# Kernel optimization log

Hardware: AMD Instinct MI355X
Metric: run time of the kernel (lower is better)

## Reference

```python
import jax, jax.numpy as jnp
import numpy as np

B, C, H, W = 2, 14, 128, 128
LOSS_WEIGHT = 0.5  # output = (1 - loss_weight) * sum of per-(bs,cls) log-Hausdorff losses
BIG = 1e6          # 'infinite' 1D distance for columns with no background pixel


def _edt_sq(is_zero):
    """Exact squared Euclidean distance transform of a [H,W] bool map.

    Returns, for every pixel, the squared distance to the nearest True pixel
    of `is_zero` (0 at True pixels). Matches scipy.ndimage.distance_transform_edt
    squared. Two-phase separable brute force (vectorized, no data loops).
    """
    h, w = is_zero.shape
    ii = jnp.arange(h, dtype=jnp.float32)
    absd = jnp.abs(ii[:, None] - ii[None, :])  # [H(i), H(p)] = |i - p|
    # d1[i, q] = min_{p : is_zero[p, q]} |i - p|   (per-column 1D distance)
    d1 = jnp.min(jnp.where(is_zero[None, :, :], absd[:, :, None], BIG), axis=1)  # [H, W]
    jj = jnp.arange(w, dtype=jnp.float32)
    off = (jj[:, None] - jj[None, :]) ** 2  # [W(q), W(j)] = (q - j)^2
    # sq[i, j] = min_q d1[i, q]^2 + (q - j)^2
    return jnp.min(d1[:, :, None] ** 2 + off[None, :, :], axis=1)  # [H, W]


def _distance_field_sq(img):
    """MONAI HausdorffDTLoss.distance_field squared: (edt(fg)+edt(bg))^2.

    fg_dist and bg_dist have disjoint supports, so (fg+bg)^2 = fg^2 + bg^2.
    Zero field if the image is all-foreground or all-background.
    """
    fg = img > 0.5
    field = _edt_sq(~fg) + _edt_sq(fg)
    valid = jnp.any(fg) & jnp.any(~fg)
    return jnp.where(valid, field, 0.0)


def _edge_mask(m):
    """mask XOR binary_erosion(mask): scipy default cross structuring element,
    border_value=0 (borders erode)."""
    p = jnp.pad(m, 1, constant_values=False)
    er = m & p[:-2, 1:-1] & p[2:, 1:-1] & p[1:-1, :-2] & p[1:-1, 2:]
    return m & ~er


def _pair_loss(stud_logit, seg_s, seg_t, teach_pred):
    # stud_logit: [H,W] float logits of this class; seg_s/seg_t: [H,W] bool
    # class masks; teach_pred: [H,W] teacher argmax labels (int)
    es = _edge_mask(seg_s).astype(stud_logit.dtype)
    et = _edge_mask(seg_t)
    pred = es * stud_logit                                      # edges * logits
    targ = jnp.where(et, teach_pred.astype(stud_logit.dtype), 0.0)  # edges * labels
    pred_dt2 = jax.lax.stop_gradient(_distance_field_sq(pred))  # MONAI detaches dt
    targ_dt2 = jax.lax.stop_gradient(_distance_field_sq(targ))
    hd = jnp.mean((pred - targ) ** 2 * (pred_dt2 + targ_dt2))   # alpha = 2
    return jnp.log(hd + 1.0)                                    # LogHausdorffDTLoss


def reference(logits_student, logits_teacher):
    ps = jnp.argmax(logits_student, axis=1)  # softmax is monotone -> argmax of logits
    pt = jnp.argmax(logits_teacher, axis=1)
    cls = jnp.arange(1, C)                   # classes 1..C-1 (background skipped)
    n = B * (C - 1)
    seg_s = (ps[:, None] == cls[None, :, None, None]).reshape(n, H, W)
    seg_t = (pt[:, None] == cls[None, :, None, None]).reshape(n, H, W)
    stud = logits_student[:, 1:].reshape(n, H, W)
    pt_rep = jnp.broadcast_to(pt[:, None], (B, C - 1, H, W)).reshape(n, H, W)
    losses = jax.vmap(_pair_loss)(stud, seg_s, seg_t, pt_rep)
    return (1.0 - LOSS_WEIGHT) * jnp.sum(losses)


def setup_inputs() -> dict:
    key = jax.random.key(0)
    k1, k2 = jax.random.split(key)
    return {
        "logits_student": jax.random.normal(k1, (B, C, H, W), dtype=jnp.float32),
        "logits_teacher": jax.random.normal(k2, (B, C, H, W), dtype=jnp.float32),
    }
```

## Files before the change

kernel.cpp:

```cpp
#include <hip/hip_runtime.h>
#include <math.h>
#include <limits.h>

#define HH 128
#define WW 128
#define HW (HH*WW)
#define BB 2
#define CC 14
#define NPAIR 26
#define RPB 8
#define NBLK (NPAIR * (HH / RPB))

typedef unsigned long long u64;


__device__ inline int nbd(u64 lo, u64 hi, int i) {
    int up = 255, down = 255;
    u64 slo, shi;
    if (i == 0)      { slo = lo; shi = hi; }
    else if (i < 64) { slo = (lo >> i) | (hi << (64 - i)); shi = hi >> i; }
    else             { slo = hi >> (i - 64); shi = 0ULL; }
    if (slo)      up = __builtin_ctzll(slo);
    else if (shi) up = 64 + __builtin_ctzll(shi);
    int s = 127 - i;
    u64 llo, lhi;
    if (s == 0)      { llo = lo; lhi = hi; }
    else if (s < 64) { lhi = (hi << s) | (lo >> (64 - s)); llo = lo << s; }
    else             { lhi = lo << (s - 64); llo = 0ULL; }
    if (lhi)      down = __builtin_clzll(lhi);
    else if (llo) down = 64 + __builtin_clzll(llo);
    return min(up, down);
}

__global__ void k_argmax(const float* __restrict__ Ls, const float* __restrict__ Lt,
                         unsigned char* __restrict__ lab, unsigned short* __restrict__ hb,
                         float* __restrict__ sums, int* __restrict__ done) {
    if (blockIdx.x == 0) {
        if (threadIdx.x < NPAIR) sums[threadIdx.x] = 0.0f;
        if (threadIdx.x == 0) *done = 0;
    }
    int p4 = blockIdx.x * blockDim.x + threadIdx.x;
    if (p4 >= BB * HW / 4) return;
    int b = p4 >> 12;
    int q4 = p4 & (HW / 4 - 1);
    const float4* bs = (const float4*)(Ls + (size_t)b * CC * HW) + q4;
    const float4* bt = (const float4*)(Lt + (size_t)b * CC * HW) + q4;
    float4 mS = bs[0], mT = bt[0];
    uchar4 iS = make_uchar4(0, 0, 0, 0), iT = make_uchar4(0, 0, 0, 0);
    ushort4 hm = make_ushort4(0, 0, 0, 0);
#pragma unroll
    for (int c = 1; c < CC; ++c) {
        float4 v = bs[(size_t)c * (HW / 4)];
        if (v.x > mS.x) { mS.x = v.x; iS.x = (unsigned char)c; }
        if (v.y > mS.y) { mS.y = v.y; iS.y = (unsigned char)c; }
        if (v.z > mS.z) { mS.z = v.z; iS.z = (unsigned char)c; }
        if (v.w > mS.w) { mS.w = v.w; iS.w = (unsigned char)c; }
        unsigned short bit = (unsigned short)(1u << (c - 1));
        if (v.x > 0.5f) hm.x |= bit;
        if (v.y > 0.5f) hm.y |= bit;
        if (v.z > 0.5f) hm.z |= bit;
        if (v.w > 0.5f) hm.w |= bit;
        float4 u = bt[(size_t)c * (HW / 4)];
        if (u.x > mT.x) { mT.x = u.x; iT.x = (unsigned char)c; }
        if (u.y > mT.y) { mT.y = u.y; iT.y = (unsigned char)c; }
        if (u.z > mT.z) { mT.z = u.z; iT.z = (unsigned char)c; }
        if (u.w > mT.w) { mT.w = u.w; iT.w = (unsigned char)c; }
    }
    uchar4 pk = make_uchar4((unsigned char)(iS.x | (iT.x << 4)),
                            (unsigned char)(iS.y | (iT.y << 4)),
                            (unsigned char)(iS.z | (iT.z << 4)),
                            (unsigned char)(iS.w | (iT.w << 4)));
    ((uchar4*)lab)[b * (HW / 4) + q4] = pk;
    ((ushort4*)hb)[b * (HW / 4) + q4] = hm;
}

__device__ inline u64 asm64(unsigned int (*p)[WW], int k0, int j) {
    return (u64)p[k0][j] | ((u64)p[k0 + 1][j] << 16)
         | ((u64)p[k0 + 2][j] << 32) | ((u64)p[k0 + 3][j] << 48);
}

__global__ __launch_bounds__(1024) void k_C(
        const unsigned char* __restrict__ lab, const unsigned short* __restrict__ hb,
        const float* __restrict__ Ls,
        float* __restrict__ sums, int* __restrict__ done, float* __restrict__ out) {
    int n = blockIdx.x >> 4;
    int t = blockIdx.x & 15;
    int tid = threadIdx.x;
    int k = tid >> 7;
    int j = tid & (WW - 1);
    int b = n / (CC - 1), c = 1 + (n - b * (CC - 1));
    const unsigned char*  LB = lab + b * HW;
    const unsigned short* HB = hb + b * HW;
    const float* Lp = Ls + (size_t)(b * CC + c) * HW;

    int i = t * RPB + k;
    float lv = Lp[i * WW + j];

    unsigned int s16 = 0, t16 = 0, h16 = 0;
    int i0 = k << 4;
    unsigned int hbit = 1u << (c - 1);
#pragma unroll
    for (int r = 0; r < 16; ++r) {
        int off = (i0 + r) * WW + j;
        unsigned int lbv = LB[off];
        if ((lbv & 15u) == (unsigned)c)  s16 |= 1u << r;
        if ((lbv >> 4)  == (unsigned)c)  t16 |= 1u << r;
        if (HB[off] & hbit)              h16 |= 1u << r;
    }
    __shared__ unsigned int pS[8][WW], pT[8][WW], pH[8][WW];
    pS[k][j] = s16; pT[k][j] = t16; pH[k][j] = h16;
    __syncthreads();

    __shared__ ulonglong2 colFP[WW], colET[WW], colES[WW];
    __shared__ int sfl[2];
    if (tid < WW) {
        u64 ms0 = asm64(pS, 0, j), ms1 = asm64(pS, 4, j);
        u64 mt0 = asm64(pT, 0, j), mt1 = asm64(pT, 4, j);
        u64 hi0 = asm64(pH, 0, j), hi1 = asm64(pH, 4, j);
        u64 Lsx = 0, Lsy = 0, Ltx = 0, Lty = 0, Rsx = 0, Rsy = 0, Rtx = 0, Rty = 0;
        if (j > 0)      { Lsx = asm64(pS, 0, j - 1); Lsy = asm64(pS, 4, j - 1);
                          Ltx = asm64(pT, 0, j - 1); Lty = asm64(pT, 4, j - 1); }
        if (j < WW - 1) { Rsx = asm64(pS, 0, j + 1); Rsy = asm64(pS, 4, j + 1);
                          Rtx = asm64(pT, 0, j + 1); Rty = asm64(pT, 4, j + 1); }

        u64 U0 = ms0 << 1, U1 = (ms1 << 1) | (ms0 >> 63);
        u64 D0 = (ms0 >> 1) | (ms1 << 63), D1 = ms1 >> 1;
        u64 er0 = ms0 & U0 & D0 & Lsx & Rsx;
        u64 er1 = ms1 & U1 & D1 & Lsy & Rsy;
        u64 es0 = ms0 & ~er0, es1 = ms1 & ~er1;

        u64 Ut0 = mt0 << 1, Ut1 = (mt1 << 1) | (mt0 >> 63);
        u64 Dt0 = (mt0 >> 1) | (mt1 << 63), Dt1 = mt1 >> 1;
        u64 ert0 = mt0 & Ut0 & Dt0 & Ltx & Rtx;
        u64 ert1 = mt1 & Ut1 & Dt1 & Lty & Rty;
        u64 et0 = mt0 & ~ert0, et1 = mt1 & ~ert1;

        u64 fp0 = es0 & hi0, fp1 = es1 & hi1;

        colFP[j] = make_ulonglong2(fp0, fp1);
        colET[j] = make_ulonglong2(et0, et1);
        colES[j] = make_ulonglong2(es0, es1);

        u64 bFgP = __ballot((fp0 | fp1) != 0ull);
        u64 bBgP = __ballot((fp0 & fp1) != ~0ull);
        u64 bFgT = __ballot((et0 | et1) != 0ull);
        u64 bBgT = __ballot((et0 & et1) != ~0ull);
        if ((tid & 63) == 0) {
            sfl[tid >> 6] = (bFgP ? 1 : 0) | (bBgP ? 2 : 0)
                          | (bFgT ? 4 : 0) | (bBgT ? 8 : 0);
        }
    }
    __syncthreads();

    ulonglong2 mP = colFP[j];
    ulonglong2 mT = colET[j];
    ulonglong2 eS = colES[j];
    int f = sfl[0] | sfl[1];
    bool aP = (f & 3) == 3, aT = (f & 12) == 12;

    int dP  = nbd(mP.x, mP.y, i);
    int dPb = nbd(~mP.x, ~mP.y, i);
    int dT  = nbd(mT.x, mT.y, i);
    int dTb = nbd(~mT.x, ~mT.y, i);

    __shared__ uchar4 sq[RPB][WW];
    sq[k][j] = make_uchar4((unsigned char)dP, (unsigned char)dPb,
                           (unsigned char)dT, (unsigned char)dTb);
    __syncthreads();

    int bP = dP * dP, bPb = dPb * dPb, bT = dT * dT, bTb = dTb * dTb;
    int need = 0;
    if (aP) need = max(bP, bPb);
    if (aT) need = max(need, max(bT, bTb));
    for (int rad = 1; rad < WW; ++rad) {
        int rr = rad * rad;
        if (rr >= need) break;
        if (j >= rad) {
            uchar4 s = sq[k][j - rad];
            bP  = min(bP,  (int)s.x * s.x + rr); bPb = min(bPb, (int)s.y * s.y + rr);
            bT  = min(bT,  (int)s.z * s.z + rr); bTb = min(bTb, (int)s.w * s.w + rr);
        }
        if (j + rad < WW) {
            uchar4 s = sq[k][j + rad];
            bP  = min(bP,  (int)s.x * s.x + rr); bPb = min(bPb, (int)s.y * s.y + rr);
            bT  = min(bT,  (int)s.z * s.z + rr); bTb = min(bTb, (int)s.w * s.w + rr);
        }
        need = 0;
        if (aP) need = max(bP, bPb);
        if (aT) need = max(need, max(bT, bTb));
    }

    float fieldP = aP ? (float)(bP + bPb) : 0.0f;
    float fieldT = aT ? (float)(bT + bTb) : 0.0f;

    bool es = ((i < 64 ? (eS.x >> i) : (eS.y >> (i - 64))) & 1ull) != 0;
    bool et = ((i < 64 ? (mT.x >> i) : (mT.y >> (i - 64))) & 1ull) != 0;
    float predv = es ? lv : 0.0f;
    float targv = et ? (float)c : 0.0f;
    float diff = predv - targv;
    float v = diff * diff * (fieldP + fieldT);

    for (int o = 32; o > 0; o >>= 1) v += __shfl_down(v, o);
    __shared__ float wsum[16];
    __shared__ int won;
    int lane = tid & 63, w = tid >> 6;
    if (lane == 0) wsum[w] = v;
    if (tid == 0) won = 0;
    __syncthreads();
    if (tid == 0) {
        float tot = 0.0f;
#pragma unroll
        for (int q = 0; q < 16; ++q) tot += wsum[q];
        atomicAdd(&sums[n], tot);
        __threadfence();
        if (atomicAdd(done, 1) == NBLK - 1) won = 1;
    }
    __syncthreads();
    if (won && tid < 64) {
        float vv = 0.0f;
        if (tid < NPAIR) {
            float hd = atomicAdd(&sums[tid], 0.0f) * (1.0f / (float)HW);
            vv = logf(hd + 1.0f);
        }
        for (int o = 32; o > 0; o >>= 1) vv += __shfl_down(vv, o);
        if (tid == 0) out[0] = 0.5f * vv;
    }
}

extern "C" void kernel_launch(void* const* d_in, const int* in_sizes, int n_in,
                              void* d_out, int out_size, void* d_ws, size_t ws_size,
                              hipStream_t stream) {
    const float* Ls = (const float*)d_in[0];
    const float* Lt = (const float*)d_in[1];
    float* out = (float*)d_out;

    char* w = (char*)d_ws;
    unsigned char*  lab  = (unsigned char*) (w);
    unsigned short* hbm  = (unsigned short*)(w + 32768);
    float*          sums = (float*)         (w + 98304);
    int*            done = (int*)           (w + 98432);

    k_argmax<<<BB * HW / 4 / 256, 256, 0, stream>>>(Ls, Lt, lab, hbm, sums, done);
    k_C<<<NBLK, 1024, 0, stream>>>(lab, hbm, Ls, sums, done, out);
}
```

Before: 72.09 us.

## Precompute per-class column bitmasks in argmax kernel for direct loading in k_C

The first kernel now turns the argmax labels and the >0.5 bits into per-class, per-column bit-packed masks (one byte per 8 rows, 16 bytes per column) and writes them to the workspace. Each k_C block then loads its column masks with single 16-byte reads instead of having all 1024 threads gather 16 label bytes each and assemble bitmasks through shared memory. This moves the per-class packing work out of the 416 k_C blocks, which repeat it for every row tile, and into the pack pass. The cost is extra scattered byte-sized global writes in the first kernel and a larger workspace.

```diff
diff --git a/kernel.cpp b/kernel.cpp
--- a/kernel.cpp
+++ b/kernel.cpp
@@ -32,15 +32,16 @@
     return min(up, down);
 }
 
-__global__ void k_argmax(const float* __restrict__ Ls, const float* __restrict__ Lt,
-                         unsigned char* __restrict__ lab, unsigned short* __restrict__ hb,
-                         float* __restrict__ sums, int* __restrict__ done) {
+__global__ void k_pack(const float* __restrict__ Ls, const float* __restrict__ Lt,
+                       unsigned char* __restrict__ Scol, unsigned char* __restrict__ Tcol,
+                       unsigned char* __restrict__ Hcol,
+                       float* __restrict__ sums, int* __restrict__ done) {
+    int tid = threadIdx.x;
     if (blockIdx.x == 0) {
-        if (threadIdx.x < NPAIR) sums[threadIdx.x] = 0.0f;
-        if (threadIdx.x == 0) *done = 0;
-    }
-    int p4 = blockIdx.x * blockDim.x + threadIdx.x;
-    if (p4 >= BB * HW / 4) return;
+        if (tid < NPAIR) sums[tid] = 0.0f;
+        if (tid == 0) *done = 0;
+    }
+    int p4 = blockIdx.x * 256 + tid;
     int b = p4 >> 12;
     int q4 = p4 & (HW / 4 - 1);
     const float4* bs = (const float4*)(Ls + (size_t)b * CC * HW) + q4;
@@ -66,22 +67,53 @@
         if (u.z > mT.z) { mT.z = u.z; iT.z = (unsigned char)c; }
         if (u.w > mT.w) { mT.w = u.w; iT.w = (unsigned char)c; }
     }
-    uchar4 pk = make_uchar4((unsigned char)(iS.x | (iT.x << 4)),
-                            (unsigned char)(iS.y | (iT.y << 4)),
-                            (unsigned char)(iS.z | (iT.z << 4)),
-                            (unsigned char)(iS.w | (iT.w << 4)));
-    ((uchar4*)lab)[b * (HW / 4) + q4] = pk;
-    ((ushort4*)hb)[b * (HW / 4) + q4] = hm;
-}
-
-__device__ inline u64 asm64(unsigned int (*p)[WW], int k0, int j) {
-    return (u64)p[k0][j] | ((u64)p[k0 + 1][j] << 16)
-         | ((u64)p[k0 + 2][j] << 32) | ((u64)p[k0 + 3][j] << 48);
+    __shared__ unsigned char  labL[8][WW];
+    __shared__ unsigned short hL[8][WW];
+    int r  = tid >> 5;
+    int c4 = (tid & 31) * 4;
+    *(uchar4*)&labL[r][c4] = make_uchar4(
+        (unsigned char)(iS.x | (iT.x << 4)), (unsigned char)(iS.y | (iT.y << 4)),
+        (unsigned char)(iS.z | (iT.z << 4)), (unsigned char)(iS.w | (iT.w << 4)));
+    *(ushort4*)&hL[r][c4] = hm;
+    __syncthreads();
+
+    int j  = tid & (WW - 1);
+    int g  = blockIdx.x & 15;
+    int n0 = b * CC;
+    if (tid < 128) {
+        unsigned char lr[8];
+#pragma unroll
+        for (int rr = 0; rr < 8; ++rr) lr[rr] = labL[rr][j];
+#pragma unroll
+        for (int cc = 1; cc < CC; ++cc) {
+            unsigned int sb = 0, tb = 0;
+#pragma unroll
+            for (int rr = 0; rr < 8; ++rr) {
+                sb |= (unsigned int)((lr[rr] & 15) == cc) << rr;
+                tb |= (unsigned int)((lr[rr] >> 4)  == cc) << rr;
+            }
+            size_t off = ((size_t)(((n0 + cc) << 7) | j) << 4) + g;
+            Scol[off] = (unsigned char)sb;
+            Tcol[off] = (unsigned char)tb;
+        }
+    } else {
+        unsigned short hr[8];
+#pragma unroll
+        for (int rr = 0; rr < 8; ++rr) hr[rr] = hL[rr][j];
+#pragma unroll
+        for (int cc = 1; cc < CC; ++cc) {
+            unsigned int hbb = 0;
+#pragma unroll
+            for (int rr = 0; rr < 8; ++rr) hbb |= ((hr[rr] >> (cc - 1)) & 1u) << rr;
+            size_t off = ((size_t)(((n0 + cc) << 7) | j) << 4) + g;
+            Hcol[off] = (unsigned char)hbb;
+        }
+    }
 }
 
 __global__ __launch_bounds__(1024) void k_C(
-        const unsigned char* __restrict__ lab, const unsigned short* __restrict__ hb,
-        const float* __restrict__ Ls,
+        const unsigned char* __restrict__ Scol, const unsigned char* __restrict__ Tcol,
+        const unsigned char* __restrict__ Hcol, const float* __restrict__ Ls,
         float* __restrict__ sums, int* __restrict__ done, float* __restrict__ out) {
     int n = blockIdx.x >> 4;
     int t = blockIdx.x & 15;
@@ -89,39 +121,32 @@
     int k = tid >> 7;
     int j = tid & (WW - 1);
     int b = n / (CC - 1), c = 1 + (n - b * (CC - 1));
-    const unsigned char*  LB = lab + b * HW;
-    const unsigned short* HB = hb + b * HW;
     const float* Lp = Ls + (size_t)(b * CC + c) * HW;
 
     int i = t * RPB + k;
     float lv = Lp[i * WW + j];
 
-    unsigned int s16 = 0, t16 = 0, h16 = 0;
-    int i0 = k << 4;
-    unsigned int hbit = 1u << (c - 1);
-#pragma unroll
-    for (int r = 0; r < 16; ++r) {
-        int off = (i0 + r) * WW + j;
-        unsigned int lbv = LB[off];
-        if ((lbv & 15u) == (unsigned)c)  s16 |= 1u << r;
-        if ((lbv >> 4)  == (unsigned)c)  t16 |= 1u << r;
-        if (HB[off] & hbit)              h16 |= 1u << r;
-    }
-    __shared__ unsigned int pS[8][WW], pT[8][WW], pH[8][WW];
-    pS[k][j] = s16; pT[k][j] = t16; pH[k][j] = h16;
-    __syncthreads();
-
+    __shared__ ulonglong2 colS[WW], colT[WW];
     __shared__ ulonglong2 colFP[WW], colET[WW], colES[WW];
     __shared__ int sfl[2];
+
+    ulonglong2 S, T, Hc;
     if (tid < WW) {
-        u64 ms0 = asm64(pS, 0, j), ms1 = asm64(pS, 4, j);
-        u64 mt0 = asm64(pT, 0, j), mt1 = asm64(pT, 4, j);
-        u64 hi0 = asm64(pH, 0, j), hi1 = asm64(pH, 4, j);
+        size_t mb = ((size_t)(((b * CC + c) << 7) | tid)) << 4;
+        S  = *(const ulonglong2*)(Scol + mb);
+        T  = *(const ulonglong2*)(Tcol + mb);
+        Hc = *(const ulonglong2*)(Hcol + mb);
+        colS[tid] = S; colT[tid] = T;
+    }
+    __syncthreads();
+
+    if (tid < WW) {
+        u64 ms0 = S.x, ms1 = S.y, mt0 = T.x, mt1 = T.y;
         u64 Lsx = 0, Lsy = 0, Ltx = 0, Lty = 0, Rsx = 0, Rsy = 0, Rtx = 0, Rty = 0;
-        if (j > 0)      { Lsx = asm64(pS, 0, j - 1); Lsy = asm64(pS, 4, j - 1);
-                          Ltx = asm64(pT, 0, j - 1); Lty = asm64(pT, 4, j - 1); }
-        if (j < WW - 1) { Rsx = asm64(pS, 0, j + 1); Rsy = asm64(pS, 4, j + 1);
-                          Rtx = asm64(pT, 0, j + 1); Rty = asm64(pT, 4, j + 1); }
+        if (j > 0)      { ulonglong2 v = colS[j - 1]; Lsx = v.x; Lsy = v.y;
+                          v = colT[j - 1]; Ltx = v.x; Lty = v.y; }
+        if (j < WW - 1) { ulonglong2 v = colS[j + 1]; Rsx = v.x; Rsy = v.y;
+                          v = colT[j + 1]; Rtx = v.x; Rty = v.y; }
 
         u64 U0 = ms0 << 1, U1 = (ms1 << 1) | (ms0 >> 63);
         u64 D0 = (ms0 >> 1) | (ms1 << 63), D1 = ms1 >> 1;
@@ -135,7 +160,7 @@
         u64 ert1 = mt1 & Ut1 & Dt1 & Lty & Rty;
         u64 et0 = mt0 & ~ert0, et1 = mt1 & ~ert1;
 
-        u64 fp0 = es0 & hi0, fp1 = es1 & hi1;
+        u64 fp0 = es0 & Hc.x, fp1 = es1 & Hc.y;
 
         colFP[j] = make_ulonglong2(fp0, fp1);
         colET[j] = make_ulonglong2(et0, et1);
@@ -235,11 +260,12 @@
     float* out = (float*)d_out;
 
     char* w = (char*)d_ws;
-    unsigned char*  lab  = (unsigned char*) (w);
-    unsigned short* hbm  = (unsigned short*)(w + 32768);
-    float*          sums = (float*)         (w + 98304);
-    int*            done = (int*)           (w + 98432);
-
-    k_argmax<<<BB * HW / 4 / 256, 256, 0, stream>>>(Ls, Lt, lab, hbm, sums, done);
-    k_C<<<NBLK, 1024, 0, stream>>>(lab, hbm, Ls, sums, done, out);
-}
+    unsigned char* Sc   = (unsigned char*)(w);
+    unsigned char* Tc   = (unsigned char*)(w + 57344);
+    unsigned char* Hc   = (unsigned char*)(w + 114688);
+    float*         sums = (float*)        (w + 172032);
+    int*           done = (int*)          (w + 172160);
+
+    k_pack<<<BB * HW / 4 / 256, 256, 0, stream>>>(Ls, Lt, Sc, Tc, Hc, sums, done);
+    k_C<<<NBLK, 1024, 0, stream>>>(Sc, Tc, Hc, Ls, sums, done, out);
+}
```

New measurement: 72.11 us. No clear change (+0.0%).
